# Kernel tuning notes

Measured on AMD Instinct MI355X. Metric: run time of the kernel, lower is better.

## Reference

```python
import jax, jax.numpy as jnp
import numpy as np

D = 1024       # hidden_size
H = 16         # num_heads
DH = D // H    # d_keys = d_values = 64
FF = int(D * 2.0)  # mlp hidden
EPS = 1e-6


def _ln(t):
    # LayerNorm, elementwise_affine=False
    mu = jnp.mean(t, axis=-1, keepdims=True)
    var = jnp.mean((t - mu) ** 2, axis=-1, keepdims=True)
    return (t - mu) * jax.lax.rsqrt(var + EPS)


def setup_inputs() -> dict:
    key = jax.random.key(0)
    ks = jax.random.split(key, 16)
    B, L = 2, 2048
    s = 0.02
    return {
        "x": jax.random.normal(ks[0], (B, L, D), jnp.float32),
        "c": jax.random.normal(ks[1], (B, 1, D), jnp.float32),
        "Wq": jax.random.normal(ks[2], (D, D), jnp.float32) * s,
        "bq": jnp.zeros((D,), jnp.float32),
        "Wk": jax.random.normal(ks[3], (D, D), jnp.float32) * s,
        "bk": jnp.zeros((D,), jnp.float32),
        "Wv": jax.random.normal(ks[4], (D, D), jnp.float32) * s,
        "bv": jnp.zeros((D,), jnp.float32),
        "Wo": jax.random.normal(ks[5], (D, D), jnp.float32) * s,
        "bo": jnp.zeros((D,), jnp.float32),
        "W1": jax.random.normal(ks[6], (D, FF), jnp.float32) * s,
        "b1": jnp.zeros((FF,), jnp.float32),
        "W2": jax.random.normal(ks[7], (FF, D), jnp.float32) * s,
        "b2": jnp.zeros((D,), jnp.float32),
        "Wada": jax.random.normal(ks[8], (D, 6 * D), jnp.float32) * s,
        "bada": jnp.zeros((6 * D,), jnp.float32),
    }


def reference(x, c, Wq, bq, Wk, bk, Wv, bv, Wo, bo, W1, b1, W2, b2, Wada, bada):
    B, L, _ = x.shape
    # adaLN-Zero modulation params (dropout layers act as identity in eval)
    ada = jax.nn.silu(c) @ Wada + bada  # [B,1,6D]
    shift_msa, scale_msa, gate_msa, shift_mlp, scale_mlp, gate_mlp = jnp.split(ada, 6, axis=-1)

    # --- attention branch ---
    h = _ln(x) * (1.0 + scale_msa) + shift_msa
    q = (h @ Wq + bq).reshape(B, L, H, DH)
    k = (h @ Wk + bk).reshape(B, L, H, DH)
    v = (h @ Wv + bv).reshape(B, L, H, DH)
    scale = 1.0 / np.sqrt(DH).astype(np.float32)
    scores = jnp.einsum('blhe,bshe->bhls', q, k)  # full LxL scores, as in source
    A = jax.nn.softmax(scale * scores, axis=-1)
    out = jnp.einsum('bhls,bshd->blhd', A, v)     # [B,L,H,DH]
    # mix=True: transpose(2,1) then view(B,L,-1) -> head/position mixing reshape
    out = jnp.transpose(out, (0, 2, 1, 3)).reshape(B, L, H * DH)
    x = x + gate_msa * (out @ Wo + bo)

    # --- MLP branch (exact GELU: nn.GELU() passed as act_layer) ---
    h2 = _ln(x) * (1.0 + scale_mlp) + shift_mlp
    m = jax.nn.gelu(h2 @ W1 + b1, approximate=False) @ W2 + b2
    return x + gate_mlp * m
```

## Files before the change

### kernel.cpp

```cpp
#include <hip/hip_runtime.h>
#include <hip/hip_bf16.h>

typedef unsigned short ushort_t;
typedef __bf16 bf16x8 __attribute__((ext_vector_type(8)));
typedef float f32x4 __attribute__((ext_vector_type(4)));

typedef unsigned int u32;
typedef u32 __attribute__((address_space(1))) global_u32;
typedef u32 __attribute__((address_space(3))) lds_u32;

#define D_ 1024
#define L_ 2048
#define B_ 2
#define H_ 16
#define DH_ 64
#define FF_ 2048
#define ADA_ 6144
#define BHL_ (B_ * H_ * L_)

#define MFMA __builtin_amdgcn_mfma_f32_16x16x32_bf16

__device__ __forceinline__ ushort_t f2bf(float f) {
    union { float f; u32 u; } v; v.f = f;
    u32 r = v.u + 0x7fffu + ((v.u >> 16) & 1u);
    return (ushort_t)(r >> 16);
}

__device__ __forceinline__ u32 pk_bf16(float a, float b) {
    float2 f; f.x = a; f.y = b;
    __hip_bfloat162 t = __float22bfloat162_rn(f);
    union { __hip_bfloat162 b2; u32 u; } v; v.b2 = t; return v.u;
}

__device__ __forceinline__ void llds16(const ushort_t* src, ushort_t* dst) {
    __builtin_amdgcn_global_load_lds((global_u32*)src, (lds_u32*)dst, 16, 0, 0);
}

__global__ void transpose_w_all(
    const float* __restrict__ Wq, const float* __restrict__ Wk,
    const float* __restrict__ Wv, const float* __restrict__ Wo,
    const float* __restrict__ W1, const float* __restrict__ W2,
    ushort_t* __restrict__ Wqkv, ushort_t* __restrict__ Wo_t,
    ushort_t* __restrict__ W1_t, ushort_t* __restrict__ W2_t) {
    __shared__ float tile[64][65];
    int id = blockIdx.x;
    const float* W; ushort_t* Wt; int K, N, ntx, lid;
    if (id < 1024) {
        int which = id >> 8; lid = id & 255; K = 1024; N = 1024; ntx = 16;
        W  = which == 0 ? Wq : which == 1 ? Wk : which == 2 ? Wv : Wo;
        Wt = which == 3 ? Wo_t : Wqkv + (size_t)which * 1024 * 1024;
    } else if (id < 1536) {
        lid = id - 1024; W = W1; Wt = W1_t; K = 1024; N = 2048; ntx = 32;
    } else {
        lid = id - 1536; W = W2; Wt = W2_t; K = 2048; N = 1024; ntx = 16;
    }
    int n0 = (lid % ntx) * 64, k0 = (lid / ntx) * 64;
    int t = threadIdx.x;
    for (int p = 0; p < 4; ++p) {
        int k = p * 16 + (t >> 4), nn = (t & 15) * 4;
        float4 v = *(const float4*)(W + (size_t)(k0 + k) * N + n0 + nn);
        tile[k][nn] = v.x; tile[k][nn + 1] = v.y; tile[k][nn + 2] = v.z; tile[k][nn + 3] = v.w;
    }
    __syncthreads();
    for (int p = 0; p < 4; ++p) {
        int n = p * 16 + (t >> 4), kk = (t & 15) * 4;
        ushort4 o;
        o.x = f2bf(tile[kk][n]); o.y = f2bf(tile[kk + 1][n]);
        o.z = f2bf(tile[kk + 2][n]); o.w = f2bf(tile[kk + 3][n]);
        *(ushort4*)(Wt + (size_t)(n0 + n) * K + k0 + kk) = o;
    }
}

__global__ void ada_gemv(const float* __restrict__ c, const float* __restrict__ Wada,
                         float* __restrict__ partial) {
    int ks = blockIdx.y;
    int j = blockIdx.x * 256 + threadIdx.x;
    __shared__ float s0[64], s1[64];
    if (threadIdx.x < 64) {
        float v = c[ks * 64 + threadIdx.x];
        s0[threadIdx.x] = v / (1.f + __expf(-v));
        v = c[D_ + ks * 64 + threadIdx.x];
        s1[threadIdx.x] = v / (1.f + __expf(-v));
    }
    __syncthreads();
    float a0 = 0.f, a1 = 0.f;
#pragma unroll 8
    for (int d = 0; d < 64; ++d) {
        float w = Wada[(size_t)(ks * 64 + d) * ADA_ + j];
        a0 = fmaf(s0[d], w, a0);
        a1 = fmaf(s1[d], w, a1);
    }
    partial[(size_t)(ks * 2 + 0) * ADA_ + j] = a0;
    partial[(size_t)(ks * 2 + 1) * ADA_ + j] = a1;
}

__global__ void ada_reduce(const float* __restrict__ partial,
                           const float* __restrict__ bada, float* __restrict__ ada) {
    int j = blockIdx.x * 256 + threadIdx.x;
    float a0 = bada[j], a1 = bada[j];
#pragma unroll
    for (int ks = 0; ks < 16; ++ks) {
        a0 += partial[(size_t)(ks * 2 + 0) * ADA_ + j];
        a1 += partial[(size_t)(ks * 2 + 1) * ADA_ + j];
    }
    ada[j] = a0;
    ada[ADA_ + j] = a1;
}

__global__ void ln_mod(const float* __restrict__ x, const float* __restrict__ ada,
                       int so, int co, ushort_t* __restrict__ out) {
    int row = blockIdx.x;
    int b = row >> 11;
    float4 v = ((const float4*)(x + (size_t)row * D_))[threadIdx.x];
    float sum = v.x + v.y + v.z + v.w;
    float sq = v.x * v.x + v.y * v.y + v.z * v.z + v.w * v.w;
    for (int off = 32; off; off >>= 1) { sum += __shfl_down(sum, off); sq += __shfl_down(sq, off); }
    __shared__ float sa[4], sb[4];
    int wave = threadIdx.x >> 6, lane = threadIdx.x & 63;
    if (lane == 0) { sa[wave] = sum; sb[wave] = sq; }
    __syncthreads();
    sum = sa[0] + sa[1] + sa[2] + sa[3];
    sq = sb[0] + sb[1] + sb[2] + sb[3];
    float mean = sum * (1.f / 1024.f);
    float var = sq * (1.f / 1024.f) - mean * mean;
    float rstd = rsqrtf(var + 1e-6f);
    int d = threadIdx.x * 4;
    const float* shf = ada + (size_t)b * ADA_ + so;
    const float* scf = ada + (size_t)b * ADA_ + co;
    uint2 ov;
    ov.x = pk_bf16((v.x - mean) * rstd * (1.f + scf[d + 0]) + shf[d + 0],
                   (v.y - mean) * rstd * (1.f + scf[d + 1]) + shf[d + 1]);
    ov.y = pk_bf16((v.z - mean) * rstd * (1.f + scf[d + 2]) + shf[d + 2],
                   (v.w - mean) * rstd * (1.f + scf[d + 3]) + shf[d + 3]);
    *(uint2*)(out + (size_t)row * D_ + d) = ov;
}

struct EpiArgs {
    const float* bias0; const float* bias1; const float* bias2;
    ushort_t* o0; ushort_t* o1; ushort_t* o2;
    const float* resid; const float* gate;
    float* fout;
};

template <int EPI>
__device__ __forceinline__ void epi_store(float v, int m, int n, int N, const EpiArgs& e) {
    if (EPI == 0) {
        int which = n >> 10, cc = n & 1023;
        const float* bias = which == 0 ? e.bias0 : e.bias1;
        ushort_t* ob = which == 0 ? e.o0 : e.o1;
        v += bias[cc];
        if (which == 0) v *= 0.18033688f;
        int b = m >> 11, l = m & 2047, h = cc >> 6, dh = cc & 63;
        ob[(((size_t)(b * H_ + h) * L_) + l) * DH_ + dh] = f2bf(v);
    } else if (EPI == 1) {
        v += e.bias0[n];
        v = 0.5f * v * (1.f + erff(v * 0.70710678118f));
        e.o0[(size_t)m * N + n] = f2bf(v);
    } else {
        int b = m >> 11;
        e.fout[(size_t)m * N + n] =
            e.resid[(size_t)m * N + n] + e.gate[(size_t)b * ADA_ + n] * (v + e.bias0[n]);
    }
}

template <int EPI>
__device__ __forceinline__ void st4(const f32x4& cc, int mb, int n, int N, const EpiArgs& e) {
    if (EPI == 0 && n >= 2048) {
        int ccn = n & 1023;
        float b4 = e.bias2[ccn];
        int b = mb >> 11, l0 = mb & 2047, h = ccn >> 6, dh = ccn & 63;
        ushort4 o;
        o.x = f2bf(cc[0] + b4); o.y = f2bf(cc[1] + b4);
        o.z = f2bf(cc[2] + b4); o.w = f2bf(cc[3] + b4);
        *(ushort4*)(e.o2 + ((size_t)(b * H_ + h) * DH_ + dh) * L_ + l0) = o;
        return;
    }
#pragma unroll
    for (int r = 0; r < 4; ++r) epi_store<EPI>(cc[r], mb + r, n, N, e);
}

template <int EPI>
__global__ __launch_bounds__(256, 2) void gemm_bt(
    const ushort_t* __restrict__ A, const ushort_t* __restrict__ Bt,
    int M, int N, int K, EpiArgs e) {
    __shared__ ushort_t As[128 * 64];
    __shared__ ushort_t Bs[128 * 64];
    int m0 = blockIdx.x * 128, n0 = blockIdx.y * 128;
    int tid = threadIdx.x, wave = tid >> 6, lane = tid & 63;
    int quad = lane >> 4, lc = lane & 15;
    int wm = (wave & 1) * 64, wn = (wave >> 1) * 64;
    int srow = lane >> 3, sg = lane & 7;
    int sw = lc & 7;

    const ushort_t* stp[8];
    ushort_t* stl[8];
#pragma unroll
    for (int i = 0; i < 8; ++i) {
        int chunk = wave * 8 + i;
        int c = chunk & 15;
        int row = c * 8 + srow;
        stp[i] = (chunk < 16 ? A + (size_t)(m0 + row) * K
                             : Bt + (size_t)(n0 + row) * K) + (sg ^ srow) * 8;
        stl[i] = (chunk < 16 ? As : Bs) + c * 512 + lane * 8;
    }

    f32x4 c00 = {}, c01 = {}, c02 = {}, c03 = {};
    f32x4 c10 = {}, c11 = {}, c12 = {}, c13 = {};
    f32x4 c20 = {}, c21 = {}, c22 = {}, c23 = {};
    f32x4 c30 = {}, c31 = {}, c32 = {}, c33 = {};

    for (int k0 = 0; k0 < K; k0 += 64) {
#pragma unroll
        for (int i = 0; i < 8; ++i) { llds16(stp[i], stl[i]); stp[i] += 64; }
        __syncthreads();
#pragma unroll
        for (int kk = 0; kk < 2; ++kk) {
            int off = ((kk * 4 + quad) ^ sw) * 8;
            bf16x8 a0 = *(const bf16x8*)&As[(wm +  0 + lc) * 64 + off];
            bf16x8 a1 = *(const bf16x8*)&As[(wm + 16 + lc) * 64 + off];
            bf16x8 a2 = *(const bf16x8*)&As[(wm + 32 + lc) * 64 + off];
            bf16x8 a3 = *(const bf16x8*)&As[(wm + 48 + lc) * 64 + off];
            bf16x8 b0 = *(const bf16x8*)&Bs[(wn +  0 + lc) * 64 + off];
            bf16x8 b1 = *(const bf16x8*)&Bs[(wn + 16 + lc) * 64 + off];
            bf16x8 b2 = *(const bf16x8*)&Bs[(wn + 32 + lc) * 64 + off];
            bf16x8 b3 = *(const bf16x8*)&Bs[(wn + 48 + lc) * 64 + off];
            c00 = MFMA(a0, b0, c00, 0, 0, 0); c01 = MFMA(a0, b1, c01, 0, 0, 0);
            c02 = MFMA(a0, b2, c02, 0, 0, 0); c03 = MFMA(a0, b3, c03, 0, 0, 0);
            c10 = MFMA(a1, b0, c10, 0, 0, 0); c11 = MFMA(a1, b1, c11, 0, 0, 0);
            c12 = MFMA(a1, b2, c12, 0, 0, 0); c13 = MFMA(a1, b3, c13, 0, 0, 0);
            c20 = MFMA(a2, b0, c20, 0, 0, 0); c21 = MFMA(a2, b1, c21, 0, 0, 0);
            c22 = MFMA(a2, b2, c22, 0, 0, 0); c23 = MFMA(a2, b3, c23, 0, 0, 0);
            c30 = MFMA(a3, b0, c30, 0, 0, 0); c31 = MFMA(a3, b1, c31, 0, 0, 0);
            c32 = MFMA(a3, b2, c32, 0, 0, 0); c33 = MFMA(a3, b3, c33, 0, 0, 0);
        }
        __syncthreads();
    }

    int mb = m0 + wm + quad * 4, nb = n0 + wn + lc;
    st4<EPI>(c00, mb +  0, nb +  0, N, e); st4<EPI>(c01, mb +  0, nb + 16, N, e);
    st4<EPI>(c02, mb +  0, nb + 32, N, e); st4<EPI>(c03, mb +  0, nb + 48, N, e);
    st4<EPI>(c10, mb + 16, nb +  0, N, e); st4<EPI>(c11, mb + 16, nb + 16, N, e);
    st4<EPI>(c12, mb + 16, nb + 32, N, e); st4<EPI>(c13, mb + 16, nb + 48, N, e);
    st4<EPI>(c20, mb + 32, nb +  0, N, e); st4<EPI>(c21, mb + 32, nb + 16, N, e);
    st4<EPI>(c22, mb + 32, nb + 32, N, e); st4<EPI>(c23, mb + 32, nb + 48, N, e);
    st4<EPI>(c30, mb + 48, nb +  0, N, e); st4<EPI>(c31, mb + 48, nb + 16, N, e);
    st4<EPI>(c32, mb + 48, nb + 32, N, e); st4<EPI>(c33, mb + 48, nb + 48, N, e);
}

template <int EPI>
__global__ __launch_bounds__(256, 2) void gemm_bt64(
    const ushort_t* __restrict__ A, const ushort_t* __restrict__ Bt,
    int M, int N, int K, EpiArgs e) {
    __shared__ ushort_t As[64 * 64];
    __shared__ ushort_t Bs[128 * 64];
    int m0 = blockIdx.x * 64, n0 = blockIdx.y * 128;
    int tid = threadIdx.x, wave = tid >> 6, lane = tid & 63;
    int quad = lane >> 4, lc = lane & 15;
    int wn = wave * 32;
    int srow = lane >> 3, sg = lane & 7;
    int sw = lc & 7;

    const ushort_t* stp[6];
    ushort_t* stl[6];
#pragma unroll
    for (int i = 0; i < 6; ++i) {
        int chunk = wave * 6 + i;
        if (chunk < 8) {
            int row = chunk * 8 + srow;
            stp[i] = A + (size_t)(m0 + row) * K + (sg ^ srow) * 8;
            stl[i] = &As[chunk * 512 + lane * 8];
        } else {
            int c = chunk - 8;
            int row = c * 8 + srow;
            stp[i] = Bt + (size_t)(n0 + row) * K + (sg ^ srow) * 8;
            stl[i] = &Bs[c * 512 + lane * 8];
        }
    }

    f32x4 c00 = {}, c01 = {};
    f32x4 c10 = {}, c11 = {};
    f32x4 c20 = {}, c21 = {};
    f32x4 c30 = {}, c31 = {};

    for (int k0 = 0; k0 < K; k0 += 64) {
#pragma unroll
        for (int i = 0; i < 6; ++i) { llds16(stp[i], stl[i]); stp[i] += 64; }
        __syncthreads();
#pragma unroll
        for (int kk = 0; kk < 2; ++kk) {
            int off = ((kk * 4 + quad) ^ sw) * 8;
            bf16x8 a0 = *(const bf16x8*)&As[( 0 + lc) * 64 + off];
            bf16x8 a1 = *(const bf16x8*)&As[(16 + lc) * 64 + off];
            bf16x8 a2 = *(const bf16x8*)&As[(32 + lc) * 64 + off];
            bf16x8 a3 = *(const bf16x8*)&As[(48 + lc) * 64 + off];
            bf16x8 b0 = *(const bf16x8*)&Bs[(wn +  0 + lc) * 64 + off];
            bf16x8 b1 = *(const bf16x8*)&Bs[(wn + 16 + lc) * 64 + off];
            c00 = MFMA(a0, b0, c00, 0, 0, 0); c01 = MFMA(a0, b1, c01, 0, 0, 0);
            c10 = MFMA(a1, b0, c10, 0, 0, 0); c11 = MFMA(a1, b1, c11, 0, 0, 0);
            c20 = MFMA(a2, b0, c20, 0, 0, 0); c21 = MFMA(a2, b1, c21, 0, 0, 0);
            c30 = MFMA(a3, b0, c30, 0, 0, 0); c31 = MFMA(a3, b1, c31, 0, 0, 0);
        }
        __syncthreads();
    }

    int mb = m0 + quad * 4, nb = n0 + wn + lc;
    st4<EPI>(c00, mb +  0, nb + 0, N, e); st4<EPI>(c01, mb +  0, nb + 16, N, e);
    st4<EPI>(c10, mb + 16, nb + 0, N, e); st4<EPI>(c11, mb + 16, nb + 16, N, e);
    st4<EPI>(c20, mb + 32, nb + 0, N, e); st4<EPI>(c21, mb + 32, nb + 16, N, e);
    st4<EPI>(c30, mb + 48, nb + 0, N, e); st4<EPI>(c31, mb + 48, nb + 16, N, e);
}

__global__ __launch_bounds__(256, 2) void attn(
    const ushort_t* __restrict__ Q, const ushort_t* __restrict__ Kx,
    const ushort_t* __restrict__ Vt, ushort_t* __restrict__ O) {
    __shared__ ushort_t Ks[128 * 64];
    __shared__ ushort_t Vs[64 * 128];
    int id = blockIdx.x;
    int bh = ((id & 7) << 2) + ((id >> 3) & 3);
    int qt = id >> 5;
    const ushort_t* Qg = Q + ((size_t)bh * L_ + qt * 128) * DH_;
    const ushort_t* Kg = Kx + (size_t)bh * L_ * DH_;
    const ushort_t* Vg = Vt + (size_t)bh * DH_ * L_;
    int tid = threadIdx.x, wave = tid >> 6, lane = tid & 63;
    int quad = lane >> 4, lc = lane & 15;
    int sw = lc & 7;
    int srow = lane >> 3, sg = lane & 7;

    const ushort_t* stp[8];
    ushort_t* stl[8];
    int stinc;
    if (wave < 2) {
        stinc = 128 * DH_;
#pragma unroll
        for (int i = 0; i < 8; ++i) {
            int chunk = wave * 8 + i;
            int slot = chunk * 8 + srow;
            int s5 = slot & 31;
            int sig = (slot & ~31) + ((s5 & 15) >> 2) * 8 + (s5 & 3) + (s5 >> 4) * 4;
            stp[i] = Kg + (size_t)sig * DH_ + (sg ^ srow) * 8;
            stl[i] = &Ks[chunk * 512 + lane * 8];
        }
    } else {
        stinc = 128;
#pragma unroll
        for (int i = 0; i < 8; ++i) {
            int c2 = (wave - 2) * 8 + i;
            int row = c2 * 4 + (lane >> 4);
            int g = (lane & 15) ^ (row & 15);
            stp[i] = Vg + (size_t)row * L_ + g * 8;
            stl[i] = &Vs[c2 * 512 + lane * 8];
        }
    }

    const ushort_t* qp = Qg + (size_t)(wave * 32 + lc) * DH_ + quad * 8;
    bf16x8 q00 = *(const bf16x8*)(qp);
    bf16x8 q01 = *(const bf16x8*)(qp + 32);
    bf16x8 q10 = *(const bf16x8*)(qp + 16 * DH_);
    bf16x8 q11 = *(const bf16x8*)(qp + 16 * DH_ + 32);

    union { u32 u[4]; bf16x8 v; } ones;
    ones.u[0] = ones.u[1] = ones.u[2] = ones.u[3] = 0x3F803F80u;

    f32x4 o00 = {}, o01 = {}, o02 = {}, o03 = {};
    f32x4 o10 = {}, o11 = {}, o12 = {}, o13 = {};
    f32x4 osum0 = {}, osum1 = {};

    for (int t = 0; t < 16; ++t) {
#pragma unroll
        for (int i = 0; i < 8; ++i) { llds16(stp[i], stl[i]); stp[i] += stinc; }
        __syncthreads();

        f32x4 s[2][8];
        __builtin_amdgcn_s_setprio(1);
#pragma unroll
        for (int kk = 0; kk < 2; ++kk) {
            int off = ((kk * 4 + quad) ^ sw) * 8;
            bf16x8 aq0 = kk == 0 ? q00 : q01;
            bf16x8 aq1 = kk == 0 ? q10 : q11;
#pragma unroll
            for (int ni = 0; ni < 8; ++ni) {
                bf16x8 bk = *(const bf16x8*)&Ks[(ni * 16 + lc) * 64 + off];
                if (kk == 0) {
                    f32x4 z = {0.f, 0.f, 0.f, 0.f};
                    s[0][ni] = MFMA(bk, aq0, z, 0, 0, 0);
                    s[1][ni] = MFMA(bk, aq1, z, 0, 0, 0);
                } else {
                    s[0][ni] = MFMA(bk, aq0, s[0][ni], 0, 0, 0);
                    s[1][ni] = MFMA(bk, aq1, s[1][ni], 0, 0, 0);
                }
            }
        }
        __builtin_amdgcn_s_setprio(0);

        u32 px[2][8], py[2][8];
#pragma unroll
        for (int pi = 0; pi < 2; ++pi) {
#pragma unroll
            for (int ni = 0; ni < 8; ++ni) {
                float p0 = __builtin_amdgcn_exp2f(s[pi][ni][0]);
                float p1 = __builtin_amdgcn_exp2f(s[pi][ni][1]);
                float p2 = __builtin_amdgcn_exp2f(s[pi][ni][2]);
                float p3 = __builtin_amdgcn_exp2f(s[pi][ni][3]);
                px[pi][ni] = pk_bf16(p0, p1);
                py[pi][ni] = pk_bf16(p2, p3);
            }
        }

        __builtin_amdgcn_s_setprio(1);
#pragma unroll
        for (int kk = 0; kk < 4; ++kk) {
            int gq = kk * 4 + quad;
            bf16x8 bv0 = *(const bf16x8*)&Vs[( 0 + lc) * 128 + ((gq ^ lc) * 8)];
            bf16x8 bv1 = *(const bf16x8*)&Vs[(16 + lc) * 128 + ((gq ^ lc) * 8)];
            bf16x8 bv2 = *(const bf16x8*)&Vs[(32 + lc) * 128 + ((gq ^ lc) * 8)];
            bf16x8 bv3 = *(const bf16x8*)&Vs[(48 + lc) * 128 + ((gq ^ lc) * 8)];
            union { u32 u[4]; bf16x8 v; } a0, a1;
            a0.u[0] = px[0][2 * kk]; a0.u[1] = py[0][2 * kk];
            a0.u[2] = px[0][2 * kk + 1]; a0.u[3] = py[0][2 * kk + 1];
            a1.u[0] = px[1][2 * kk]; a1.u[1] = py[1][2 * kk];
            a1.u[2] = px[1][2 * kk + 1]; a1.u[3] = py[1][2 * kk + 1];
            o00 = MFMA(a0.v, bv0, o00, 0, 0, 0); o01 = MFMA(a0.v, bv1, o01, 0, 0, 0);
            o02 = MFMA(a0.v, bv2, o02, 0, 0, 0); o03 = MFMA(a0.v, bv3, o03, 0, 0, 0);
            o10 = MFMA(a1.v, bv0, o10, 0, 0, 0); o11 = MFMA(a1.v, bv1, o11, 0, 0, 0);
            o12 = MFMA(a1.v, bv2, o12, 0, 0, 0); o13 = MFMA(a1.v, bv3, o13, 0, 0, 0);
            osum0 = MFMA(a0.v, ones.v, osum0, 0, 0, 0);
            osum1 = MFMA(a1.v, ones.v, osum1, 0, 0, 0);
        }
        __builtin_amdgcn_s_setprio(0);
        __syncthreads();
    }

    f32x4 inv0, inv1;
#pragma unroll
    for (int r = 0; r < 4; ++r) { inv0[r] = 1.f / osum0[r]; inv1[r] = 1.f / osum1[r]; }
#pragma unroll
    for (int pi = 0; pi < 2; ++pi) {
        const f32x4& iv = pi == 0 ? inv0 : inv1;
#pragma unroll
        for (int nio = 0; nio < 4; ++nio) {
            const f32x4& ov = pi == 0 ? (nio == 0 ? o00 : nio == 1 ? o01 : nio == 2 ? o02 : o03)
                                      : (nio == 0 ? o10 : nio == 1 ? o11 : nio == 2 ? o12 : o13);
#pragma unroll
            for (int r = 0; r < 4; ++r) {
                int row = qt * 128 + wave * 32 + pi * 16 + quad * 4 + r;
                O[((size_t)bh * L_ + row) * DH_ + nio * 16 + lc] = f2bf(ov[r] * iv[r]);
            }
        }
    }
}

extern "C" void kernel_launch(void* const* d_in, const int* in_sizes, int n_in,
                              void* d_out, int out_size, void* d_ws, size_t ws_size,
                              hipStream_t stream) {
    (void)in_sizes; (void)n_in; (void)out_size; (void)ws_size;
    const float* x    = (const float*)d_in[0];
    const float* c    = (const float*)d_in[1];
    const float* Wq   = (const float*)d_in[2];
    const float* bq   = (const float*)d_in[3];
    const float* Wk   = (const float*)d_in[4];
    const float* bk   = (const float*)d_in[5];
    const float* Wv   = (const float*)d_in[6];
    const float* bv   = (const float*)d_in[7];
    const float* Wo   = (const float*)d_in[8];
    const float* bo   = (const float*)d_in[9];
    const float* W1   = (const float*)d_in[10];
    const float* b1   = (const float*)d_in[11];
    const float* W2   = (const float*)d_in[12];
    const float* b2   = (const float*)d_in[13];
    const float* Wada = (const float*)d_in[14];
    const float* bada = (const float*)d_in[15];

    char* w = (char*)d_ws;
    float*    ada  = (float*)(w + 0);
    ushort_t* Wqkv = (ushort_t*)(w + 49152);
    ushort_t* Wo_t = (ushort_t*)(w + 6340608);
    ushort_t* W1_t = (ushort_t*)(w + 8437760);
    ushort_t* W2_t = (ushort_t*)(w + 12632064);
    ushort_t* h    = (ushort_t*)(w + 16826368);
    ushort_t* Qb   = (ushort_t*)(w + 25214976);
    ushort_t* Kb   = (ushort_t*)(w + 33603584);
    ushort_t* Ob   = (ushort_t*)(w + 41992192);
    ushort_t* Vtb  = (ushort_t*)(w + 50380800);
    float*    x1   = (float*)(w + 58769408);
    ushort_t* m1   = Qb;
    float*    adap = (float*)Vtb;

    const int M = B_ * L_;

    transpose_w_all<<<2048, 256, 0, stream>>>(Wq, Wk, Wv, Wo, W1, W2,
                                              Wqkv, Wo_t, W1_t, W2_t);

    ada_gemv<<<dim3(24, 16), 256, 0, stream>>>(c, Wada, adap);
    ada_reduce<<<24, 256, 0, stream>>>(adap, bada, ada);
    ln_mod<<<M, 256, 0, stream>>>(x, ada, 0, 1024, h);

    EpiArgs e0 = {bq, bk, bv, Qb, Kb, Vtb, nullptr, nullptr, nullptr};
    gemm_bt<0><<<dim3(32, 24), 256, 0, stream>>>(h, Wqkv, M, 3072, D_, e0);

    attn<<<512, 256, 0, stream>>>(Qb, Kb, Vtb, Ob);

    EpiArgs e1 = {bo, nullptr, nullptr, nullptr, nullptr, nullptr, x, ada + 2048, x1};
    gemm_bt64<2><<<dim3(64, 8), 256, 0, stream>>>(Ob, Wo_t, M, D_, D_, e1);

    ln_mod<<<M, 256, 0, stream>>>(x1, ada, 3072, 4096, h);

    EpiArgs e2 = {b1, nullptr, nullptr, m1, nullptr, nullptr, nullptr, nullptr, nullptr};
    gemm_bt64<1><<<dim3(64, 16), 256, 0, stream>>>(h, W1_t, M, FF_, D_, e2);

    EpiArgs e3 = {b2, nullptr, nullptr, nullptr, nullptr, nullptr, x1, ada + 5120, (float*)d_out};
    gemm_bt64<2><<<dim3(64, 8), 256, 0, stream>>>(m1, W2_t, M, D_, FF_, e3);
}
```

Before: 314.7 us.

## Split attention query tile across eight waves with sixteen rows each

```diff
diff --git a/kernel.cpp b/kernel.cpp
--- a/kernel.cpp
+++ b/kernel.cpp
@@ -310,7 +310,7 @@
     st4<EPI>(c30, mb + 48, nb + 0, N, e); st4<EPI>(c31, mb + 48, nb + 16, N, e);
 }
 
-__global__ __launch_bounds__(256, 2) void attn(
+__global__ __launch_bounds__(512, 4) void attn(
     const ushort_t* __restrict__ Q, const ushort_t* __restrict__ Kx,
     const ushort_t* __restrict__ Vt, ushort_t* __restrict__ O) {
     __shared__ ushort_t Ks[128 * 64];
@@ -326,14 +326,14 @@
     int sw = lc & 7;
     int srow = lane >> 3, sg = lane & 7;
 
-    const ushort_t* stp[8];
-    ushort_t* stl[8];
+    const ushort_t* stp[4];
+    ushort_t* stl[4];
     int stinc;
-    if (wave < 2) {
+    if (wave < 4) {
         stinc = 128 * DH_;
 #pragma unroll
-        for (int i = 0; i < 8; ++i) {
-            int chunk = wave * 8 + i;
+        for (int i = 0; i < 4; ++i) {
+            int chunk = wave * 4 + i;
             int slot = chunk * 8 + srow;
             int s5 = slot & 31;
             int sig = (slot & ~31) + ((s5 & 15) >> 2) * 8 + (s5 & 3) + (s5 >> 4) * 4;
@@ -343,8 +343,8 @@
     } else {
         stinc = 128;
 #pragma unroll
-        for (int i = 0; i < 8; ++i) {
-            int c2 = (wave - 2) * 8 + i;
+        for (int i = 0; i < 4; ++i) {
+            int c2 = (wave - 4) * 4 + i;
             int row = c2 * 4 + (lane >> 4);
             int g = (lane & 15) ^ (row & 15);
             stp[i] = Vg + (size_t)row * L_ + g * 8;
@@ -352,58 +352,49 @@
         }
     }
 
-    const ushort_t* qp = Qg + (size_t)(wave * 32 + lc) * DH_ + quad * 8;
-    bf16x8 q00 = *(const bf16x8*)(qp);
-    bf16x8 q01 = *(const bf16x8*)(qp + 32);
-    bf16x8 q10 = *(const bf16x8*)(qp + 16 * DH_);
-    bf16x8 q11 = *(const bf16x8*)(qp + 16 * DH_ + 32);
+    const ushort_t* qp = Qg + (size_t)(wave * 16 + lc) * DH_ + quad * 8;
+    bf16x8 q0 = *(const bf16x8*)(qp);
+    bf16x8 q1 = *(const bf16x8*)(qp + 32);
 
     union { u32 u[4]; bf16x8 v; } ones;
     ones.u[0] = ones.u[1] = ones.u[2] = ones.u[3] = 0x3F803F80u;
 
-    f32x4 o00 = {}, o01 = {}, o02 = {}, o03 = {};
-    f32x4 o10 = {}, o11 = {}, o12 = {}, o13 = {};
-    f32x4 osum0 = {}, osum1 = {};
+    f32x4 o0 = {}, o1 = {}, o2 = {}, o3 = {};
+    f32x4 osum = {};
 
     for (int t = 0; t < 16; ++t) {
 #pragma unroll
-        for (int i = 0; i < 8; ++i) { llds16(stp[i], stl[i]); stp[i] += stinc; }
-        __syncthreads();
-
-        f32x4 s[2][8];
+        for (int i = 0; i < 4; ++i) { llds16(stp[i], stl[i]); stp[i] += stinc; }
+        __syncthreads();
+
+        f32x4 s[8];
         __builtin_amdgcn_s_setprio(1);
 #pragma unroll
         for (int kk = 0; kk < 2; ++kk) {
             int off = ((kk * 4 + quad) ^ sw) * 8;
-            bf16x8 aq0 = kk == 0 ? q00 : q01;
-            bf16x8 aq1 = kk == 0 ? q10 : q11;
+            bf16x8 aq = kk == 0 ? q0 : q1;
 #pragma unroll
             for (int ni = 0; ni < 8; ++ni) {
                 bf16x8 bk = *(const bf16x8*)&Ks[(ni * 16 + lc) * 64 + off];
                 if (kk == 0) {
                     f32x4 z = {0.f, 0.f, 0.f, 0.f};
-                    s[0][ni] = MFMA(bk, aq0, z, 0, 0, 0);
-                    s[1][ni] = MFMA(bk, aq1, z, 0, 0, 0);
+                    s[ni] = MFMA(bk, aq, z, 0, 0, 0);
                 } else {
-                    s[0][ni] = MFMA(bk, aq0, s[0][ni], 0, 0, 0);
-                    s[1][ni] = MFMA(bk, aq1, s[1][ni], 0, 0, 0);
+                    s[ni] = MFMA(bk, aq, s[ni], 0, 0, 0);
                 }
             }
         }
         __builtin_amdgcn_s_setprio(0);
 
-        u32 px[2][8], py[2][8];
-#pragma unroll
-        for (int pi = 0; pi < 2; ++pi) {
-#pragma unroll
-            for (int ni = 0; ni < 8; ++ni) {
-                float p0 = __builtin_amdgcn_exp2f(s[pi][ni][0]);
-                float p1 = __builtin_amdgcn_exp2f(s[pi][ni][1]);
-                float p2 = __builtin_amdgcn_exp2f(s[pi][ni][2]);
-                float p3 = __builtin_amdgcn_exp2f(s[pi][ni][3]);
-                px[pi][ni] = pk_bf16(p0, p1);
-                py[pi][ni] = pk_bf16(p2, p3);
-            }
+        u32 px[8], py[8];
+#pragma unroll
+        for (int ni = 0; ni < 8; ++ni) {
+            float p0 = __builtin_amdgcn_exp2f(s[ni][0]);
+            float p1 = __builtin_amdgcn_exp2f(s[ni][1]);
+            float p2 = __builtin_amdgcn_exp2f(s[ni][2]);
+            float p3 = __builtin_amdgcn_exp2f(s[ni][3]);
+            px[ni] = pk_bf16(p0, p1);
+            py[ni] = pk_bf16(p2, p3);
         }
 
         __builtin_amdgcn_s_setprio(1);
@@ -414,37 +405,27 @@
             bf16x8 bv1 = *(const bf16x8*)&Vs[(16 + lc) * 128 + ((gq ^ lc) * 8)];
             bf16x8 bv2 = *(const bf16x8*)&Vs[(32 + lc) * 128 + ((gq ^ lc) * 8)];
             bf16x8 bv3 = *(const bf16x8*)&Vs[(48 + lc) * 128 + ((gq ^ lc) * 8)];
-            union { u32 u[4]; bf16x8 v; } a0, a1;
-            a0.u[0] = px[0][2 * kk]; a0.u[1] = py[0][2 * kk];
-            a0.u[2] = px[0][2 * kk + 1]; a0.u[3] = py[0][2 * kk + 1];
-            a1.u[0] = px[1][2 * kk]; a1.u[1] = py[1][2 * kk];
-            a1.u[2] = px[1][2 * kk + 1]; a1.u[3] = py[1][2 * kk + 1];
-            o00 = MFMA(a0.v, bv0, o00, 0, 0, 0); o01 = MFMA(a0.v, bv1, o01, 0, 0, 0);
-            o02 = MFMA(a0.v, bv2, o02, 0, 0, 0); o03 = MFMA(a0.v, bv3, o03, 0, 0, 0);
-            o10 = MFMA(a1.v, bv0, o10, 0, 0, 0); o11 = MFMA(a1.v, bv1, o11, 0, 0, 0);
-            o12 = MFMA(a1.v, bv2, o12, 0, 0, 0); o13 = MFMA(a1.v, bv3, o13, 0, 0, 0);
-            osum0 = MFMA(a0.v, ones.v, osum0, 0, 0, 0);
-            osum1 = MFMA(a1.v, ones.v, osum1, 0, 0, 0);
+            union { u32 u[4]; bf16x8 v; } a;
+            a.u[0] = px[2 * kk]; a.u[1] = py[2 * kk];
+            a.u[2] = px[2 * kk + 1]; a.u[3] = py[2 * kk + 1];
+            o0 = MFMA(a.v, bv0, o0, 0, 0, 0); o1 = MFMA(a.v, bv1, o1, 0, 0, 0);
+            o2 = MFMA(a.v, bv2, o2, 0, 0, 0); o3 = MFMA(a.v, bv3, o3, 0, 0, 0);
+            osum = MFMA(a.v, ones.v, osum, 0, 0, 0);
         }
         __builtin_amdgcn_s_setprio(0);
         __syncthreads();
     }
 
-    f32x4 inv0, inv1;
-#pragma unroll
-    for (int r = 0; r < 4; ++r) { inv0[r] = 1.f / osum0[r]; inv1[r] = 1.f / osum1[r]; }
-#pragma unroll
-    for (int pi = 0; pi < 2; ++pi) {
-        const f32x4& iv = pi == 0 ? inv0 : inv1;
-#pragma unroll
-        for (int nio = 0; nio < 4; ++nio) {
-            const f32x4& ov = pi == 0 ? (nio == 0 ? o00 : nio == 1 ? o01 : nio == 2 ? o02 : o03)
-                                      : (nio == 0 ? o10 : nio == 1 ? o11 : nio == 2 ? o12 : o13);
-#pragma unroll
-            for (int r = 0; r < 4; ++r) {
-                int row = qt * 128 + wave * 32 + pi * 16 + quad * 4 + r;
-                O[((size_t)bh * L_ + row) * DH_ + nio * 16 + lc] = f2bf(ov[r] * iv[r]);
-            }
+    f32x4 inv;
+#pragma unroll
+    for (int r = 0; r < 4; ++r) inv[r] = 1.f / osum[r];
+#pragma unroll
+    for (int nio = 0; nio < 4; ++nio) {
+        const f32x4& ov = nio == 0 ? o0 : nio == 1 ? o1 : nio == 2 ? o2 : o3;
+#pragma unroll
+        for (int r = 0; r < 4; ++r) {
+            int row = qt * 128 + wave * 16 + quad * 4 + r;
+            O[((size_t)bh * L_ + row) * DH_ + nio * 16 + lc] = f2bf(ov[r] * inv[r]);
         }
     }
 }
@@ -497,7 +478,7 @@
     EpiArgs e0 = {bq, bk, bv, Qb, Kb, Vtb, nullptr, nullptr, nullptr};
     gemm_bt<0><<<dim3(32, 24), 256, 0, stream>>>(h, Wqkv, M, 3072, D_, e0);
 
-    attn<<<512, 256, 0, stream>>>(Qb, Kb, Vtb, Ob);
+    attn<<<512, 512, 0, stream>>>(Qb, Kb, Vtb, Ob);
 
     EpiArgs e1 = {bo, nullptr, nullptr, nullptr, nullptr, nullptr, x, ada + 2048, x1};
     gemm_bt64<2><<<dim3(64, 8), 256, 0, stream>>>(Ob, Wo_t, M, D_, D_, e1);
```

New measurement: 309.2 us (median of 2 runs). No clear change (-1.7%).
